# Kernel optimization log

Measured on AMD Instinct MI355X. Metric: run time of the kernel, lower is better.

The kernel has to match this reference:

```python
import jax, jax.numpy as jnp
import numpy as np

TEMPERATURE = 0.07
BASE_TEMPERATURE = 0.07
ANCHOR_NUM = 256   # total_classes after hard-anchor sampling
N_VIEW = 16
FEAT_DIM = 256
NUM_CLASSES = 19


def setup_inputs() -> dict:
    key = jax.random.key(0)
    k1, k2 = jax.random.split(key)
    feats = jax.random.normal(k1, (ANCHOR_NUM, N_VIEW, FEAT_DIM), dtype=jnp.float32)
    # projection-head outputs are L2-normalized in the upstream network
    feats = feats / jnp.linalg.norm(feats, axis=-1, keepdims=True)
    labels = jax.random.randint(k2, (ANCHOR_NUM,), 0, NUM_CLASSES, dtype=jnp.int32)
    return {"feats": feats, "labels": labels}


def reference(feats, labels) -> jnp.ndarray:
    # feats: [A, V, D] sampled anchors; labels: [A] class ids
    A, V, D = feats.shape
    N = A * V
    dt = feats.dtype
    # torch.cat(torch.unbind(feats_, dim=1), dim=0) -> view-major ordering
    contrast = feats.transpose(1, 0, 2).reshape(N, D)          # [N, D]
    lbl = jnp.tile(labels, V)                                   # [N]

    logits = jnp.matmul(contrast, contrast.T) / jnp.asarray(TEMPERATURE, dt)  # [N, N]
    logits = logits - jax.lax.stop_gradient(jnp.max(logits, axis=1, keepdims=True))

    pos_mask = (lbl[:, None] == lbl[None, :]).astype(dt)        # [N, N]
    neg_mask = 1.0 - pos_mask
    diag = jnp.arange(N)
    pos_mask = pos_mask.at[diag, diag].set(0.0)                 # drop self-contrast

    exp_logits = jnp.exp(logits)
    neg_sum = jnp.sum(exp_logits * neg_mask, axis=1, keepdims=True)  # [N, 1]
    log_prob = logits - jnp.log(exp_logits + neg_sum)
    mean_log_prob_pos = jnp.sum(pos_mask * log_prob, axis=1) / jnp.sum(pos_mask, axis=1)
    loss = -(TEMPERATURE / BASE_TEMPERATURE) * mean_log_prob_pos
    return jnp.mean(loss)
```

## Files before the change

kernel.cpp:

```cpp
#include <hip/hip_runtime.h>
#include <hip/hip_bf16.h>

#define D_DIM   256
#define N_TOT   4096
#define N_ANCH  256
#define NGRP    32
#define NOFF    496
#define NBLK    512
#define NPART   64
#define K1  20.60992915555662f
#define LN2 0.6931471805599453f
#define MAXNP    48

typedef __attribute__((ext_vector_type(8))) short bf16x8;
typedef __attribute__((ext_vector_type(4))) float f32x4;

#define MFMA(a, b, c) __builtin_amdgcn_mfma_f32_16x16x32_bf16((a), (b), (c), 0, 0, 0)

__device__ __forceinline__ bf16x8 cvt8(const float4 a, const float4 b) {
    union { uint32_t w[4]; bf16x8 v; } u;
    asm("v_cvt_pk_bf16_f32 %0, %1, %2" : "=v"(u.w[0]) : "v"(a.x), "v"(a.y));
    asm("v_cvt_pk_bf16_f32 %0, %1, %2" : "=v"(u.w[1]) : "v"(a.z), "v"(a.w));
    asm("v_cvt_pk_bf16_f32 %0, %1, %2" : "=v"(u.w[2]) : "v"(b.x), "v"(b.y));
    asm("v_cvt_pk_bf16_f32 %0, %1, %2" : "=v"(u.w[3]) : "v"(b.z), "v"(b.w));
    return u.v;
}

__global__ void __launch_bounds__(256, 2) k_pass1(const float* __restrict__ feats,
                                                  const int* __restrict__ labels,
                                                  float* __restrict__ partAll,
                                                  float* __restrict__ posBuf,
                                                  float* __restrict__ out) {
    __shared__ __align__(16) char lds[65536];
    __shared__ int labS[N_ANCH];
    __shared__ int cntS[32];
    __shared__ int metaRank[16], metaToff[16];

    if (blockIdx.x == 0 && threadIdx.x == 0) out[0] = 0.f;

    const int tid = threadIdx.x;
    const int lane = tid & 63, wid = tid >> 6;
    const int lrow = lane & 15, khalf = lane >> 4;
    const int wr = wid >> 1, wc = wid & 1;

    labS[tid] = labels[tid];
    if (tid < 32) cntS[tid] = 0;
    __syncthreads();
    atomicAdd(&cntS[labS[tid]], 1);

    uint32_t LgF[8], Lw[8];
#pragma unroll
    for (int o = 0; o < 8; ++o) {
        uint32_t L = (uint32_t)(tid * 16 + o * 4096);
        LgF[o] = (L >> 8) * 1024 + ((L & 255) << 1);
        Lw[o]  = L ^ (((L >> 8) & 7u) << 4);
    }
    const uint32_t swz = (uint32_t)((lrow & 7) << 4);

    auto gemm_tile = [&](int g, int s) {
        const bool diag = (g == s);
        const char* aSrcF = (const char*)(feats + (size_t)g * 128 * D_DIM);
        const char* bSrcF = (const char*)(feats + (size_t)s * 128 * D_DIM);
        const uint32_t bBase = diag ? 0u : 32768u;

        f32x4 acc[4][4];
#pragma unroll
        for (int m = 0; m < 4; ++m)
#pragma unroll
            for (int n = 0; n < 4; ++n)
                acc[m][n] = (f32x4){0.f, 0.f, 0.f, 0.f};

        auto compute = [&]() {
#pragma unroll
            for (int ks = 0; ks < 4; ++ks) {
                bf16x8 af[4], bfr[4];
#pragma unroll
                for (int m = 0; m < 4; ++m) {
                    uint32_t row = (uint32_t)(wr * 64 + m * 16 + lrow);
                    af[m] = *(const bf16x8*)(lds + ((row * 256 + ks * 64 + khalf * 16) ^ swz));
                }
#pragma unroll
                for (int n = 0; n < 4; ++n) {
                    uint32_t row = (uint32_t)(wc * 64 + n * 16 + lrow);
                    bfr[n] = *(const bf16x8*)(lds + bBase + ((row * 256 + ks * 64 + khalf * 16) ^ swz));
                }
#pragma unroll
                for (int m = 0; m < 4; ++m)
#pragma unroll
                    for (int n = 0; n < 4; ++n)
                        acc[m][n] = MFMA(af[m], bfr[n], acc[m][n]);
            }
        };

        {
            float4 fa[8][2], fb[8][2];
#pragma unroll
            for (int o = 0; o < 8; ++o) {
                const char* pa = aSrcF + LgF[o];
                fa[o][0] = *(const float4*)pa;  fa[o][1] = *(const float4*)(pa + 16);
            }
            if (!diag) {
#pragma unroll
                for (int o = 0; o < 8; ++o) {
                    const char* pb = bSrcF + LgF[o];
                    fb[o][0] = *(const float4*)pb;  fb[o][1] = *(const float4*)(pb + 16);
                }
            }
#pragma unroll
            for (int o = 0; o < 8; ++o)
                *(bf16x8*)(lds + Lw[o]) = cvt8(fa[o][0], fa[o][1]);
            if (!diag) {
#pragma unroll
                for (int o = 0; o < 8; ++o)
                    *(bf16x8*)(lds + 32768 + Lw[o]) = cvt8(fb[o][0], fb[o][1]);
            }
        }
        __syncthreads();

        float4 pfa[8][2];
#pragma unroll
        for (int o = 0; o < 8; ++o) {
            const char* pa = aSrcF + LgF[o] + 512;
            pfa[o][0] = *(const float4*)pa;  pfa[o][1] = *(const float4*)(pa + 16);
        }

        {
            int aIdx = tid >> 4, q = tid & 15;
            int aAnchor = (aIdx < 8) ? (g * 8 + aIdx) : (s * 8 + aIdx - 8);
            int la = labS[aAnchor];
            int rk = 0, tf = 0;
            for (int b = q; b < aAnchor; b += 16) {
                int lb = labS[b];
                rk += (lb == la);
                tf += cntS[lb];
            }
#pragma unroll
            for (int msk = 1; msk < 16; msk <<= 1) {
                rk += __shfl_xor(rk, msk, 64);
                tf += __shfl_xor(tf, msk, 64);
            }
            if (q == 0) { metaRank[aIdx] = rk; metaToff[aIdx] = tf; }
        }

        compute();
        __syncthreads();

#pragma unroll
        for (int o = 0; o < 8; ++o)
            *(bf16x8*)(lds + Lw[o]) = cvt8(pfa[o][0], pfa[o][1]);
        if (!diag) {
            float4 fb[8][2];
#pragma unroll
            for (int o = 0; o < 8; ++o) {
                const char* pb = bSrcF + LgF[o] + 512;
                fb[o][0] = *(const float4*)pb;  fb[o][1] = *(const float4*)(pb + 16);
            }
#pragma unroll
            for (int o = 0; o < 8; ++o)
                *(bf16x8*)(lds + 32768 + Lw[o]) = cvt8(fb[o][0], fb[o][1]);
        }
        __syncthreads();
        compute();
        __syncthreads();

        const int raBase = g * 8 + wr * 4, caBase = s * 8 + wc * 4;
        int labR[4], offR[4], rankR[4], labC[4], rankC[4], offC[4];
#pragma unroll
        for (int m = 0; m < 4; ++m) {
            labR[m]  = labS[raBase + m];
            offR[m]  = metaToff[wr * 4 + m];
            rankR[m] = metaRank[wr * 4 + m];
        }
#pragma unroll
        for (int n = 0; n < 4; ++n) {
            labC[n]  = labS[caBase + n];
            rankC[n] = metaRank[8 + wc * 4 + n];
            offC[n]  = metaToff[8 + wc * 4 + n];
        }

        float aAll[4][4];
        float colP[4];
#pragma unroll
        for (int m = 0; m < 4; ++m)
#pragma unroll
            for (int i = 0; i < 4; ++i) aAll[m][i] = 0.f;
#pragma unroll
        for (int n = 0; n < 4; ++n) colP[n] = 0.f;

        float* scr = (float*)lds + wid * 256;

#pragma unroll
        for (int m = 0; m < 4; ++m) {
#pragma unroll
            for (int n = 0; n < 4; ++n) {
                f32x4 c = acc[m][n];
                float e[4];
#pragma unroll
                for (int i = 0; i < 4; ++i) {
                    e[i] = exp2f(__builtin_fmaf(c[i], K1, -K1));
                    aAll[m][i] += e[i];
                }
                if (!diag)
                    colP[n] += e[0] + e[1] + e[2] + e[3];
                if (labR[m] == labC[n]) {
                    *(f32x4*)(posBuf + (size_t)(offR[m] + rankC[n]) * 256 + lane * 4) = c;
                    if (!diag) {
#pragma unroll
                        for (int i = 0; i < 4; ++i)
                            scr[(khalf * 4 + i) * 16 + lrow] = c[i];
                        __builtin_amdgcn_s_waitcnt(0);
                        f32x4 tr = *(f32x4*)(scr + lrow * 16 + khalf * 4);
                        *(f32x4*)(posBuf + (size_t)(offC[n] + rankR[m]) * 256 + lane * 4) = tr;
                    }
                }
            }
        }

#pragma unroll
        for (int msk = 1; msk < 16; msk <<= 1)
#pragma unroll
            for (int m = 0; m < 4; ++m)
#pragma unroll
                for (int i = 0; i < 4; ++i)
                    aAll[m][i] += __shfl_xor(aAll[m][i], msk, 64);

        if (lrow == 0) {
#pragma unroll
            for (int m = 0; m < 4; ++m)
#pragma unroll
                for (int i = 0; i < 4; ++i) {
                    int row = g * 128 + wr * 64 + m * 16 + khalf * 4 + i;
                    partAll[row * NPART + s * 2 + wc] = aAll[m][i];
                }
        }

        if (!diag) {
#pragma unroll
            for (int msk = 16; msk < 64; msk <<= 1)
#pragma unroll
                for (int n = 0; n < 4; ++n)
                    colP[n] += __shfl_xor(colP[n], msk, 64);
            if (lane < 16) {
#pragma unroll
                for (int n = 0; n < 4; ++n) {
                    int row = s * 128 + wc * 64 + n * 16 + lane;
                    partAll[row * NPART + g * 2 + wr] = colP[n];
                }
            }
        }
        __syncthreads();
    };

    if (blockIdx.x < NOFF) {
        int swzId = (blockIdx.x & 7) * 62 + (blockIdx.x >> 3);
        int rem = swzId, g = 0;
        while (rem >= NGRP - 1 - g) { rem -= NGRP - 1 - g; ++g; }
        gemm_tile(g, g + 1 + rem);
    } else {
        int j = blockIdx.x - NOFF;
        gemm_tile(2 * j, 2 * j);
        gemm_tile(2 * j + 1, 2 * j + 1);
    }
}

__global__ void __launch_bounds__(256) k_passB(const float* __restrict__ posBuf,
                                               const int* __restrict__ labels,
                                               const float* __restrict__ partAll,
                                               float* __restrict__ out) {
    int rt  = blockIdx.x;
    int tid = threadIdx.x;
    int l = tid >> 2, i = tid & 3;
    int r   = (l >> 4) * 4 + i;
    int col = l & 15;
    int row16 = tid >> 4;
    int q16   = tid & 15;

    __shared__ float tile[MAXNP * 256];
    __shared__ float shA[16][17];
    __shared__ float shB[16][17];
    __shared__ float nsSh[16], PSh[16];
    __shared__ int labS[N_ANCH];
    __shared__ int cntS[32];
    __shared__ int wRk[4], wTf[4];
    __shared__ int mNp, mOff, mRank;

    labS[tid] = labels[tid];
    if (tid < 32) cntS[tid] = 0;
    __syncthreads();
    atomicAdd(&cntS[labS[tid]], 1);
    __syncthreads();
    {
        int la = labS[rt];
        int rk = 0, tf = 0;
        if (tid < rt) { int lb = labS[tid]; rk = (lb == la) ? 1 : 0; tf = cntS[lb]; }
#pragma unroll
        for (int msk = 1; msk < 64; msk <<= 1) {
            rk += __shfl_xor(rk, msk, 64);
            tf += __shfl_xor(tf, msk, 64);
        }
        if ((tid & 63) == 0) { wRk[tid >> 6] = rk; wTf[tid >> 6] = tf; }
        __syncthreads();
        if (tid == 0) {
            mNp   = cntS[la];
            mRank = wRk[0] + wRk[1] + wRk[2] + wRk[3];
            mOff  = wTf[0] + wTf[1] + wTf[2] + wTf[3];
        }
        __syncthreads();
    }
    int np = mNp, off = mOff, selfRank = mRank;

    float sE = 0.f, sP = 0.f;
    const float* src = posBuf + (size_t)off * 256 + tid;
    for (int j = 0; j < np; ++j) {
        float c = src[j * 256];
        float l2 = __builtin_fmaf(c, K1, -K1);
        float e = exp2f(l2);
        tile[j * 256 + tid] = e;
        sE += e;
        bool diag = (j == selfRank) & (col == r);
        sP += diag ? 0.f : l2;
    }
    shA[r][col] = sE;
    shB[r][col] = sP;
    __syncthreads();

    {
        const float* pa = partAll + (size_t)(rt * 16 + row16) * NPART + q16 * 4;
        float4 v = *(const float4*)pa;
        float sall = v.x + v.y + v.z + v.w;
        float e = shA[row16][q16];
        float p = shB[row16][q16];
#pragma unroll
        for (int msk = 1; msk < 16; msk <<= 1) {
            sall += __shfl_xor(sall, msk, 64);
            e    += __shfl_xor(e,    msk, 64);
            p    += __shfl_xor(p,    msk, 64);
        }
        if (q16 == 0) { nsSh[row16] = sall - e; PSh[row16] = p; }
    }
    __syncthreads();

    float nsv = nsSh[r];
    float sL = 0.f;
    for (int j = 0; j < np; ++j) {
        float e = tile[j * 256 + tid];
        float lg = __log2f(e + nsv);
        bool diag = (j == selfRank) & (col == r);
        sL += diag ? 0.f : lg;
    }
    __syncthreads();
    shA[r][col] = sL;
    __syncthreads();

    {
        float L = shA[row16][q16];
#pragma unroll
        for (int msk = 1; msk < 16; msk <<= 1)
            L += __shfl_xor(L, msk, 64);
        if (q16 == 0)
            shB[0][row16] = (PSh[row16] - L) / (float)(16 * np - 1);
    }
    __syncthreads();
    if (tid == 0) {
        float sx = 0.f;
#pragma unroll
        for (int q = 0; q < 16; ++q) sx += shB[0][q];
        atomicAdd(out, -sx * (LN2 / (float)N_TOT));
    }
}

extern "C" void kernel_launch(void* const* d_in, const int* in_sizes, int n_in,
                              void* d_out, int out_size, void* d_ws, size_t ws_size,
                              hipStream_t stream) {
    const float* feats  = (const float*)d_in[0];
    const int*   labels = (const int*)d_in[1];
    float* out = (float*)d_out;

    char* ws = (char*)d_ws;
    float*  partAll = (float*)(ws + (2u << 20));
    float*  posBuf  = (float*)(ws + (3u << 20));

    k_pass1<<<NBLK, 256, 0, stream>>>(feats, labels, partAll, posBuf, out);
    k_passB<<<N_ANCH, 256, 0, stream>>>(posBuf, labels, partAll, out);
}
```

Measured before the change: 30.49 us.

## Accumulate only negative-pair exp sums in GEMM pass and fuse passB loops

The GEMM epilogue now computes exp only for tiles whose row and column anchor labels differ, producing negative sums directly instead of all-pair sums. The later pass therefore no longer subtracts the positive exps, which lets it drop the large LDS tile buffer and merge its two loops over positive pairs into one. The transpose scratch moves to a separate LDS array so a barrier after the MFMA compute can be removed. The price is 4 KB more LDS in pass1 and a divergent branch between the exp path and the positive-pair store path.

```diff
diff --git a/kernel.cpp b/kernel.cpp
--- a/kernel.cpp
+++ b/kernel.cpp
@@ -28,10 +28,11 @@
 
 __global__ void __launch_bounds__(256, 2) k_pass1(const float* __restrict__ feats,
                                                   const int* __restrict__ labels,
-                                                  float* __restrict__ partAll,
+                                                  float* __restrict__ partNeg,
                                                   float* __restrict__ posBuf,
                                                   float* __restrict__ out) {
     __shared__ __align__(16) char lds[65536];
+    __shared__ float scrS[1024];
     __shared__ int labS[N_ANCH];
     __shared__ int cntS[32];
     __shared__ int metaRank[16], metaToff[16];
@@ -161,7 +162,6 @@
         }
         __syncthreads();
         compute();
-        __syncthreads();
 
         const int raBase = g * 8 + wr * 4, caBase = s * 8 + wc * 4;
         int labR[4], offR[4], rankR[4], labC[4], rankC[4], offC[4];
@@ -178,30 +178,22 @@
             offC[n]  = metaToff[8 + wc * 4 + n];
         }
 
-        float aAll[4][4];
+        float aNeg[4][4];
         float colP[4];
 #pragma unroll
         for (int m = 0; m < 4; ++m)
 #pragma unroll
-            for (int i = 0; i < 4; ++i) aAll[m][i] = 0.f;
+            for (int i = 0; i < 4; ++i) aNeg[m][i] = 0.f;
 #pragma unroll
         for (int n = 0; n < 4; ++n) colP[n] = 0.f;
 
-        float* scr = (float*)lds + wid * 256;
+        float* scr = scrS + wid * 256;
 
 #pragma unroll
         for (int m = 0; m < 4; ++m) {
 #pragma unroll
             for (int n = 0; n < 4; ++n) {
                 f32x4 c = acc[m][n];
-                float e[4];
-#pragma unroll
-                for (int i = 0; i < 4; ++i) {
-                    e[i] = exp2f(__builtin_fmaf(c[i], K1, -K1));
-                    aAll[m][i] += e[i];
-                }
-                if (!diag)
-                    colP[n] += e[0] + e[1] + e[2] + e[3];
                 if (labR[m] == labC[n]) {
                     *(f32x4*)(posBuf + (size_t)(offR[m] + rankC[n]) * 256 + lane * 4) = c;
                     if (!diag) {
@@ -212,6 +204,15 @@
                         f32x4 tr = *(f32x4*)(scr + lrow * 16 + khalf * 4);
                         *(f32x4*)(posBuf + (size_t)(offC[n] + rankR[m]) * 256 + lane * 4) = tr;
                     }
+                } else {
+                    float e[4];
+#pragma unroll
+                    for (int i = 0; i < 4; ++i) {
+                        e[i] = exp2f(__builtin_fmaf(c[i], K1, -K1));
+                        aNeg[m][i] += e[i];
+                    }
+                    if (!diag)
+                        colP[n] += e[0] + e[1] + e[2] + e[3];
                 }
             }
         }
@@ -222,7 +223,7 @@
             for (int m = 0; m < 4; ++m)
 #pragma unroll
                 for (int i = 0; i < 4; ++i)
-                    aAll[m][i] += __shfl_xor(aAll[m][i], msk, 64);
+                    aNeg[m][i] += __shfl_xor(aNeg[m][i], msk, 64);
 
         if (lrow == 0) {
 #pragma unroll
@@ -230,7 +231,7 @@
 #pragma unroll
                 for (int i = 0; i < 4; ++i) {
                     int row = g * 128 + wr * 64 + m * 16 + khalf * 4 + i;
-                    partAll[row * NPART + s * 2 + wc] = aAll[m][i];
+                    partNeg[row * NPART + s * 2 + wc] = aNeg[m][i];
                 }
         }
 
@@ -244,7 +245,7 @@
 #pragma unroll
                 for (int n = 0; n < 4; ++n) {
                     int row = s * 128 + wc * 64 + n * 16 + lane;
-                    partAll[row * NPART + g * 2 + wr] = colP[n];
+                    partNeg[row * NPART + g * 2 + wr] = colP[n];
                 }
             }
         }
@@ -265,7 +266,7 @@
 
 __global__ void __launch_bounds__(256) k_passB(const float* __restrict__ posBuf,
                                                const int* __restrict__ labels,
-                                               const float* __restrict__ partAll,
+                                               const float* __restrict__ partNeg,
                                                float* __restrict__ out) {
     int rt  = blockIdx.x;
     int tid = threadIdx.x;
@@ -275,10 +276,9 @@
     int row16 = tid >> 4;
     int q16   = tid & 15;
 
-    __shared__ float tile[MAXNP * 256];
     __shared__ float shA[16][17];
     __shared__ float shB[16][17];
-    __shared__ float nsSh[16], PSh[16];
+    __shared__ float nsSh[16];
     __shared__ int labS[N_ANCH];
     __shared__ int cntS[32];
     __shared__ int wRk[4], wTf[4];
@@ -305,66 +305,53 @@
             mRank = wRk[0] + wRk[1] + wRk[2] + wRk[3];
             mOff  = wTf[0] + wTf[1] + wTf[2] + wTf[3];
         }
-        __syncthreads();
-    }
+    }
+
+    {
+        const float* pa = partNeg + (size_t)(rt * 16 + row16) * NPART + q16 * 4;
+        float4 v = *(const float4*)pa;
+        float ns = v.x + v.y + v.z + v.w;
+#pragma unroll
+        for (int msk = 1; msk < 16; msk <<= 1)
+            ns += __shfl_xor(ns, msk, 64);
+        if (q16 == 0) nsSh[row16] = ns;
+    }
+    __syncthreads();
+
     int np = mNp, off = mOff, selfRank = mRank;
-
-    float sE = 0.f, sP = 0.f;
+    float nsv = nsSh[r];
+
+    float sP = 0.f, sL = 0.f;
     const float* src = posBuf + (size_t)off * 256 + tid;
     for (int j = 0; j < np; ++j) {
         float c = src[j * 256];
         float l2 = __builtin_fmaf(c, K1, -K1);
         float e = exp2f(l2);
-        tile[j * 256 + tid] = e;
-        sE += e;
-        bool diag = (j == selfRank) & (col == r);
-        sP += diag ? 0.f : l2;
-    }
-    shA[r][col] = sE;
-    shB[r][col] = sP;
+        float lg = __log2f(e + nsv);
+        bool dg = (j == selfRank) & (col == r);
+        sP += dg ? 0.f : l2;
+        sL += dg ? 0.f : lg;
+    }
+    shA[r][col] = sP;
+    shB[r][col] = sL;
     __syncthreads();
 
     {
-        const float* pa = partAll + (size_t)(rt * 16 + row16) * NPART + q16 * 4;
-        float4 v = *(const float4*)pa;
-        float sall = v.x + v.y + v.z + v.w;
-        float e = shA[row16][q16];
-        float p = shB[row16][q16];
+        float P = shA[row16][q16];
+        float L = shB[row16][q16];
 #pragma unroll
         for (int msk = 1; msk < 16; msk <<= 1) {
-            sall += __shfl_xor(sall, msk, 64);
-            e    += __shfl_xor(e,    msk, 64);
-            p    += __shfl_xor(p,    msk, 64);
-        }
-        if (q16 == 0) { nsSh[row16] = sall - e; PSh[row16] = p; }
-    }
-    __syncthreads();
-
-    float nsv = nsSh[r];
-    float sL = 0.f;
-    for (int j = 0; j < np; ++j) {
-        float e = tile[j * 256 + tid];
-        float lg = __log2f(e + nsv);
-        bool diag = (j == selfRank) & (col == r);
-        sL += diag ? 0.f : lg;
-    }
-    __syncthreads();
-    shA[r][col] = sL;
-    __syncthreads();
-
-    {
-        float L = shA[row16][q16];
-#pragma unroll
-        for (int msk = 1; msk < 16; msk <<= 1)
+            P += __shfl_xor(P, msk, 64);
             L += __shfl_xor(L, msk, 64);
+        }
         if (q16 == 0)
-            shB[0][row16] = (PSh[row16] - L) / (float)(16 * np - 1);
+            nsSh[row16] = (P - L) / (float)(16 * np - 1);
     }
     __syncthreads();
     if (tid == 0) {
         float sx = 0.f;
 #pragma unroll
-        for (int q = 0; q < 16; ++q) sx += shB[0][q];
+        for (int q = 0; q < 16; ++q) sx += nsSh[q];
         atomicAdd(out, -sx * (LN2 / (float)N_TOT));
     }
 }
@@ -377,9 +364,9 @@
     float* out = (float*)d_out;
 
     char* ws = (char*)d_ws;
-    float*  partAll = (float*)(ws + (2u << 20));
+    float*  partNeg = (float*)(ws + (2u << 20));
     float*  posBuf  = (float*)(ws + (3u << 20));
 
-    k_pass1<<<NBLK, 256, 0, stream>>>(feats, labels, partAll, posBuf, out);
-    k_passB<<<N_ANCH, 256, 0, stream>>>(posBuf, labels, partAll, out);
+    k_pass1<<<NBLK, 256, 0, stream>>>(feats, labels, partNeg, posBuf, out);
+    k_passB<<<N_ANCH, 256, 0, stream>>>(posBuf, labels, partNeg, out);
 }
```

After: 32.13 us. +5.4%, slower.
